# Kernel tuning notes

Hardware: AMD Instinct MI355X
Metric: run time of the kernel (lower is better)

## Reference

```python
import jax, jax.numpy as jnp
import numpy as np

N_IN, N_REC, T, BATCH = 128, 512, 1000, 64
ALPHA = 0.2
SIGMA = float(np.sqrt(2.0 / ALPHA) * 0.05)  # sqrt(2/alpha)*sigma_rec
EI_RATIO = 0.8
W_REC_GAIN = 1.0


def setup_inputs() -> dict:
    key = jax.random.key(0)
    k_x, k_n = jax.random.split(key)
    rng = np.random.RandomState(0)
    # w_in init: randn/sqrt(n_in)
    w_in = (rng.randn(N_IN, N_REC) / np.sqrt(N_IN)).astype(np.float32)
    # w_rec init 'randgauss' with Dale's law: abs, inhibitory rows scaled
    n_ex = int(N_REC * EI_RATIO)
    w_rec0 = W_REC_GAIN * rng.randn(N_REC, N_REC) / np.sqrt(N_REC)
    w_rec0 = np.abs(w_rec0)
    w_rec0[n_ex:, :] *= EI_RATIO / (1.0 - EI_RATIO)
    w_rec = w_rec0.astype(np.float32)
    ei_vec = np.concatenate([np.ones(n_ex), -np.ones(N_REC - n_ex)]).astype(np.float32)
    ei_mask = np.diag(ei_vec)
    autapse_mask = np.ones((N_REC, N_REC), dtype=np.float32)
    np.fill_diagonal(autapse_mask, 0.0)
    x = jax.random.normal(k_x, (BATCH, T, N_IN), dtype=jnp.float32)
    # pre-scaled noise: randn * sigma, one draw per timestep (matches torch.randn_like(h)*sigma)
    noise = jax.random.normal(k_n, (BATCH, T, N_REC), dtype=jnp.float32) * SIGMA
    return {
        "x": x,
        "w_in": jnp.asarray(w_in),
        "w_rec": jnp.asarray(w_rec),
        "b_rec": jnp.zeros((N_REC,), dtype=jnp.float32),
        "ei_mask": jnp.asarray(ei_mask),
        "autapse_mask": jnp.asarray(autapse_mask),
        "noise": noise,
    }


def reference(x, w_in, w_rec, b_rec, ei_mask, autapse_mask, noise):
    # Effective recurrent weight, computed ONCE (torch code recomputes each step)
    w_eff = ei_mask @ (w_rec * autapse_mask)          # (n_rec, n_rec)
    inp_all = jnp.einsum("bti,ir->btr", x, w_in)       # precompute input projection
    xs = (jnp.swapaxes(inp_all, 0, 1), jnp.swapaxes(noise, 0, 1))  # (T,b,r)
    h0 = jnp.zeros((x.shape[0], w_rec.shape[0]), dtype=x.dtype)

    def step(h, xt):
        inp_t, noise_t = xt
        pre = inp_t + h @ w_eff + b_rec + noise_t
        h_new = (1.0 - ALPHA) * h + ALPHA * jax.nn.relu(pre)
        return h_new, h_new

    _, h_all = jax.lax.scan(step, h0, xs)              # (T, batch, n_rec)
    return jnp.swapaxes(h_all, 0, 1)                   # (batch, T, n_rec)
```

## Files before the change

### kernel.cpp

```cpp
#include <hip/hip_runtime.h>

#define T_STEPS 1000
#define NIN     128
#define NREC    512
#define NBATCH  64
#define ALPHA   0.2f

#define NSLICE  4
#define SCOLS   128
#define NGRP    8
#define KPER    64

#define WS_W_OFF      0
#define WS_COMM_OFF   (1u << 20)
#define COMM_U64      (NBATCH * NREC)
#define COMM_BYTES    (2 * COMM_U64 * 8)
#define WS_COMM2_OFF  (WS_COMM_OFF + COMM_BYTES)
#define WS_NEEDED_LLC (WS_COMM_OFF + COMM_BYTES)
#define WS_NEEDED_DUAL (WS_COMM2_OFF + COMM_BYTES)

#define LDS_BARRIER() do {                                        \
    asm volatile("s_waitcnt lgkmcnt(0)" ::: "memory");            \
    __builtin_amdgcn_s_barrier();                                 \
    asm volatile("" ::: "memory");                                \
} while (0)

__device__ __forceinline__ unsigned long long ld_l2(
        const unsigned long long* p) {
    unsigned long long r;
    asm volatile("global_load_dwordx2 %0, %1, off sc0\n\t"
                 "s_waitcnt vmcnt(0)"
                 : "=v"(r) : "v"(p) : "memory");
    return r;
}
__device__ __forceinline__ void st_l2(unsigned long long* p,
                                      unsigned long long v) {
    asm volatile("global_store_dwordx2 %0, %1, off"
                 :: "v"(p), "v"(v) : "memory");
}
__device__ __forceinline__ unsigned long long ld_llc(
        const unsigned long long* p) {
    return __hip_atomic_load(p, __ATOMIC_RELAXED, __HIP_MEMORY_SCOPE_AGENT);
}
__device__ __forceinline__ void st_llc(unsigned long long* p,
                                       unsigned long long v) {
    __hip_atomic_store(p, v, __ATOMIC_RELAXED, __HIP_MEMORY_SCOPE_AGENT);
}

__global__ void weff_kernel(const float* __restrict__ w_rec,
                            const float* __restrict__ ei_mask,
                            const float* __restrict__ autapse,
                            float* __restrict__ w_eff) {
    int idx = blockIdx.x * blockDim.x + threadIdx.x;
    if (idx < NREC * NREC) {
        int row = idx >> 9;
        float ei = ei_mask[row * NREC + row];
        w_eff[idx] = ei * w_rec[idx] * autapse[idx];
    }
}

__global__ __launch_bounds__(1024) void gemm_in_kernel(
        const float* __restrict__ x,
        const float* __restrict__ w_in,
        const float* __restrict__ b_rec,
        float* __restrict__ io) {
    __shared__ float xs[32][NIN];

    const int tid = threadIdx.x;
    const int m0  = blockIdx.x * 32;

    {
        const float4* src = reinterpret_cast<const float4*>(x + (size_t)m0 * NIN);
        reinterpret_cast<float4*>(&xs[0][0])[tid] = src[tid];
    }
    __syncthreads();

    const int j0 = tid & 255;
    const int j1 = j0 + 256;
    const int rg = tid >> 8;

    float acc[8][2];
#pragma unroll
    for (int i = 0; i < 8; ++i) { acc[i][0] = 0.f; acc[i][1] = 0.f; }

#pragma unroll 4
    for (int k = 0; k < NIN; ++k) {
        float wv0 = w_in[k * NREC + j0];
        float wv1 = w_in[k * NREC + j1];
#pragma unroll
        for (int i = 0; i < 8; ++i) {
            float xv = xs[rg * 8 + i][k];
            acc[i][0] = fmaf(xv, wv0, acc[i][0]);
            acc[i][1] = fmaf(xv, wv1, acc[i][1]);
        }
    }

    const float br0 = b_rec[j0];
    const float br1 = b_rec[j1];
#pragma unroll
    for (int i = 0; i < 8; ++i) {
        size_t ro = (size_t)(m0 + rg * 8 + i) * NREC;
        io[ro + j0] = acc[i][0] + br0;
        io[ro + j1] = acc[i][1] + br1;
    }
}

__global__ __launch_bounds__(1024, 4) void rnn_coop(
        const float* __restrict__ W,
        const float* __restrict__ noise,
        float* __restrict__ io,
        unsigned long long* __restrict__ comm,
        unsigned long long* __restrict__ comm2) {
    __shared__ float h_own[SCOLS];
    __shared__ float part[NGRP][SCOLS];

    const int tid = threadIdx.x;
    const int bid = blockIdx.x;
    const int b   = (bid & 7) + 8 * (bid >> 5);
    const int s   = (bid >> 3) & 3;
    const int w   = tid >> 6;
    const int ln  = tid & 63;
    const int g   = w >> 1;
    const int c   = w & 1;
    const int col = c * 64 + ln;
    const int jg  = s * SCOLS + col;
    const bool own       = (w >> 2) == s;
    const bool is_leader = own && ((w & 2) == 0);
    const bool use_l2    = (comm2 != nullptr);

    float Wr[KPER];
    {
        const float* wp = W + (size_t)(g * KPER) * NREC + jg;
#pragma unroll
        for (int u = 0; u < KPER; ++u)
            Wr[u] = wp[(size_t)u * NREC];
    }
#pragma unroll
    for (int u = 0; u < KPER; ++u)
        asm volatile("" : "+v"(Wr[u]));

    float hj = 0.f;
    const size_t iobase = (size_t)b * T_STEPS * NREC + jg;
    const unsigned long long* cpoll  = comm  + (size_t)b * NREC + g * KPER + ln;
    const unsigned long long* cpoll2 = comm2 + (size_t)b * NREC + g * KPER + ln;
    unsigned long long* cwr  = comm  + (size_t)b * NREC + jg;
    unsigned long long* cwr2 = comm2 + (size_t)b * NREC + jg;

    float inp = 0.f, nz = 0.f;
    if (is_leader) { inp = io[iobase]; nz = noise[iobase]; }

    for (int t = 0; t < T_STEPS; ++t) {
        float hval;
        if (t == 0) {
            hval = 0.f;
        } else if (own) {
            hval = h_own[(g & 1) * KPER + ln];
        } else {
            const size_t po = (size_t)(t & 1) * COMM_U64;
            unsigned long long v;
            if (use_l2) {
                v = ld_l2(cpoll2 + po);
                while ((int)(unsigned)(v >> 32) < t) {
                    v = ld_llc(cpoll + po);
                    if ((int)(unsigned)(v >> 32) >= t) break;
                    v = ld_l2(cpoll2 + po);
                }
            } else {
                v = ld_llc(cpoll + po);
                while ((int)(unsigned)(v >> 32) < t)
                    v = ld_llc(cpoll + po);
            }
            hval = __uint_as_float((unsigned)(v & 0xffffffffu));
        }

        float a0 = 0.f, a1 = 0.f;
#pragma unroll
        for (int u = 0; u < KPER; u += 2) {
            float h0 = __uint_as_float(
                __builtin_amdgcn_readlane(__float_as_uint(hval), u));
            float h1 = __uint_as_float(
                __builtin_amdgcn_readlane(__float_as_uint(hval), u + 1));
            a0 = fmaf(h0, Wr[u],     a0);
            a1 = fmaf(h1, Wr[u + 1], a1);
        }
        part[g][col] = a0 + a1;
        LDS_BARRIER();

        if (is_leader) {
            float pre = inp + nz;
#pragma unroll
            for (int q = 0; q < NGRP; ++q)
                pre += part[q][col];
            float hnew = (1.f - ALPHA) * hj + ALPHA * fmaxf(pre, 0.f);
            hj = hnew;
            h_own[col] = hnew;
            unsigned long long pv =
                ((unsigned long long)(unsigned)(t + 1) << 32) |
                (unsigned long long)__float_as_uint(hnew);
            const size_t po = (size_t)((t + 1) & 1) * COMM_U64;
            if (use_l2) st_l2(cwr2 + po, pv);
            st_llc(cwr + po, pv);
            io[iobase + (size_t)t * NREC] = hnew;
            if (t + 1 < T_STEPS) {
                inp = io[iobase + (size_t)(t + 1) * NREC];
                nz  = noise[iobase + (size_t)(t + 1) * NREC];
            }
        }
        LDS_BARRIER();
    }
}

__global__ __launch_bounds__(1024) void rnn_kernel(
        const float* __restrict__ W,
        const float* __restrict__ noise,
        float* __restrict__ io) {
    __shared__ float h[NREC];
    __shared__ float part2[NREC];

    const int tid  = threadIdx.x;
    const int j    = tid & (NREC - 1);
    const int half = tid >> 9;
    const int b    = blockIdx.x;

    if (tid < NREC) h[tid] = 0.f;
    float hj = 0.f;
    __syncthreads();

    const int kb = half * 256;
    const float* wp = W + (size_t)kb * NREC + j;
    const size_t base = (size_t)b * T_STEPS * NREC + j;

    for (int t = 0; t < T_STEPS; ++t) {
        const size_t off = base + (size_t)t * NREC;
        float acc = (half == 0) ? (io[off] + noise[off]) : 0.f;
#pragma unroll
        for (int ku = 0; ku < 256; ku += 16) {
            float wv[16];
#pragma unroll
            for (int u = 0; u < 16; ++u) wv[u] = wp[(size_t)(ku + u) * NREC];
#pragma unroll
            for (int u = 0; u < 16; ++u) acc = fmaf(h[kb + ku + u], wv[u], acc);
        }
        if (half == 1) part2[j] = acc;
        __syncthreads();
        if (half == 0) {
            float pre  = acc + part2[j];
            float hnew = (1.f - ALPHA) * hj + ALPHA * fmaxf(pre, 0.f);
            io[off] = hnew;
            h[j] = hnew;
            hj = hnew;
        }
        __syncthreads();
    }
}

extern "C" void kernel_launch(void* const* d_in, const int* in_sizes, int n_in,
                              void* d_out, int out_size, void* d_ws, size_t ws_size,
                              hipStream_t stream) {
    const float* x       = (const float*)d_in[0];
    const float* w_in    = (const float*)d_in[1];
    const float* w_rec   = (const float*)d_in[2];
    const float* b_rec   = (const float*)d_in[3];
    const float* ei_mask = (const float*)d_in[4];
    const float* autapse = (const float*)d_in[5];
    const float* noise   = (const float*)d_in[6];
    float* out = (float*)d_out;

    char* ws = (char*)d_ws;
    float* W = (float*)(ws + WS_W_OFF);
    unsigned long long* comm  = (unsigned long long*)(ws + WS_COMM_OFF);
    unsigned long long* comm2 = (unsigned long long*)(ws + WS_COMM2_OFF);

    weff_kernel<<<dim3((NREC * NREC + 255) / 256), dim3(256), 0, stream>>>(
        w_rec, ei_mask, autapse, W);

    gemm_in_kernel<<<dim3(64000 / 32), dim3(1024), 0, stream>>>(
        x, w_in, b_rec, out);

    if (ws_size >= (size_t)WS_NEEDED_DUAL) {
        hipMemsetAsync(comm, 0, 2 * COMM_BYTES, stream);
        void* args[] = {(void*)&W, (void*)&noise, (void*)&out,
                        (void*)&comm, (void*)&comm2};
        hipLaunchCooperativeKernel(reinterpret_cast<void*>(rnn_coop),
                                   dim3(NBATCH * NSLICE), dim3(1024),
                                   args, 0, stream);
    } else if (ws_size >= (size_t)WS_NEEDED_LLC) {
        hipMemsetAsync(comm, 0, COMM_BYTES, stream);
        unsigned long long* nul = nullptr;
        void* args[] = {(void*)&W, (void*)&noise, (void*)&out,
                        (void*)&comm, (void*)&nul};
        hipLaunchCooperativeKernel(reinterpret_cast<void*>(rnn_coop),
                                   dim3(NBATCH * NSLICE), dim3(1024),
                                   args, 0, stream);
    } else {
        rnn_kernel<<<dim3(NBATCH), dim3(1024), 0, stream>>>(W, noise, out);
    }
}
```

Baseline: 1.676 ms.

## Replace per-step workgroup barriers with LDS flag-based point-to-point sync

Drops both s_barrier calls per timestep in the cooperative RNN kernel and instead double-buffers the partial sums and owned hidden state in LDS. Waves signal completion through per-wave LDS flags, and leader waves spin on those flags. The waves that produced an h slice reuse their own register value, and the next-step input and noise loads are issued before the leader waits. The goal is to cut barrier stalls on the serial critical path, at the cost of LDS spin-polling and reliance on relaxed LDS atomics for correct ordering.

```diff
diff --git a/kernel.cpp b/kernel.cpp
--- a/kernel.cpp
+++ b/kernel.cpp
@@ -19,12 +19,6 @@
 #define WS_NEEDED_LLC (WS_COMM_OFF + COMM_BYTES)
 #define WS_NEEDED_DUAL (WS_COMM2_OFF + COMM_BYTES)
 
-#define LDS_BARRIER() do {                                        \
-    asm volatile("s_waitcnt lgkmcnt(0)" ::: "memory");            \
-    __builtin_amdgcn_s_barrier();                                 \
-    asm volatile("" ::: "memory");                                \
-} while (0)
-
 __device__ __forceinline__ unsigned long long ld_l2(
         const unsigned long long* p) {
     unsigned long long r;
@@ -45,6 +39,9 @@
 __device__ __forceinline__ void st_llc(unsigned long long* p,
                                        unsigned long long v) {
     __hip_atomic_store(p, v, __ATOMIC_RELAXED, __HIP_MEMORY_SCOPE_AGENT);
+}
+__device__ __forceinline__ int ld_lds_i32(const int* p) {
+    return __hip_atomic_load(p, __ATOMIC_RELAXED, __HIP_MEMORY_SCOPE_WORKGROUP);
 }
 
 __global__ void weff_kernel(const float* __restrict__ w_rec,
@@ -111,8 +108,10 @@
         float* __restrict__ io,
         unsigned long long* __restrict__ comm,
         unsigned long long* __restrict__ comm2) {
-    __shared__ float h_own[SCOLS];
-    __shared__ float part[NGRP][SCOLS];
+    __shared__ float h_own[2][SCOLS];
+    __shared__ float part[2][NGRP][SCOLS];
+    __shared__ int   wflag[2][16];
+    __shared__ int   hflag[2][2];
 
     const int tid = threadIdx.x;
     const int bid = blockIdx.x;
@@ -124,8 +123,9 @@
     const int c   = w & 1;
     const int col = c * 64 + ln;
     const int jg  = s * SCOLS + col;
-    const bool own       = (w >> 2) == s;
+    const bool own       = (g >> 1) == s;
     const bool is_leader = own && ((w & 2) == 0);
+    const bool self_h    = is_leader && (c == 0);
     const bool use_l2    = (comm2 != nullptr);
 
     float Wr[KPER];
@@ -146,17 +146,27 @@
     unsigned long long* cwr  = comm  + (size_t)b * NREC + jg;
     unsigned long long* cwr2 = comm2 + (size_t)b * NREC + jg;
 
+    if (tid < 32) wflag[tid >> 4][tid & 15] = -1;
+    if (tid < 4)  hflag[tid >> 1][tid & 1] = 0;
     float inp = 0.f, nz = 0.f;
     if (is_leader) { inp = io[iobase]; nz = noise[iobase]; }
+    __syncthreads();
 
     for (int t = 0; t < T_STEPS; ++t) {
+        const int p = t & 1;
+
         float hval;
         if (t == 0) {
             hval = 0.f;
+        } else if (self_h) {
+            hval = hj;
         } else if (own) {
-            hval = h_own[(g & 1) * KPER + ln];
+            const int need = g & 1;
+            while (ld_lds_i32(&hflag[p][need]) < t) {}
+            asm volatile("" ::: "memory");
+            hval = h_own[p][need * 64 + ln];
         } else {
-            const size_t po = (size_t)(t & 1) * COMM_U64;
+            const size_t po = (size_t)p * COMM_U64;
             unsigned long long v;
             if (use_l2) {
                 v = ld_l2(cpoll2 + po);
@@ -183,30 +193,42 @@
             a0 = fmaf(h0, Wr[u],     a0);
             a1 = fmaf(h1, Wr[u + 1], a1);
         }
-        part[g][col] = a0 + a1;
-        LDS_BARRIER();
+
+        part[p][g][col] = a0 + a1;
+        asm volatile("s_waitcnt lgkmcnt(0)" ::: "memory");
+        if (ln == 0) wflag[p][w] = t;
 
         if (is_leader) {
+            float ninp = 0.f, nnz = 0.f;
+            if (t + 1 < T_STEPS) {
+                ninp = io[iobase + (size_t)(t + 1) * NREC];
+                nnz  = noise[iobase + (size_t)(t + 1) * NREC];
+            }
+            for (;;) {
+                int fv = ld_lds_i32(&wflag[p][ln & 15]);
+                if (__all(fv >= t)) break;
+            }
+            asm volatile("" ::: "memory");
             float pre = inp + nz;
 #pragma unroll
             for (int q = 0; q < NGRP; ++q)
-                pre += part[q][col];
+                pre += part[p][q][col];
             float hnew = (1.f - ALPHA) * hj + ALPHA * fmaxf(pre, 0.f);
             hj = hnew;
-            h_own[col] = hnew;
-            unsigned long long pv =
-                ((unsigned long long)(unsigned)(t + 1) << 32) |
-                (unsigned long long)__float_as_uint(hnew);
-            const size_t po = (size_t)((t + 1) & 1) * COMM_U64;
-            if (use_l2) st_l2(cwr2 + po, pv);
-            st_llc(cwr + po, pv);
+            if (t + 1 < T_STEPS) {
+                h_own[p ^ 1][col] = hnew;
+                asm volatile("s_waitcnt lgkmcnt(0)" ::: "memory");
+                if (ln == 0) hflag[p ^ 1][c] = t + 1;
+                unsigned long long pv =
+                    ((unsigned long long)(unsigned)(t + 1) << 32) |
+                    (unsigned long long)__float_as_uint(hnew);
+                const size_t po = (size_t)((t + 1) & 1) * COMM_U64;
+                if (use_l2) st_l2(cwr2 + po, pv);
+                st_llc(cwr + po, pv);
+            }
             io[iobase + (size_t)t * NREC] = hnew;
-            if (t + 1 < T_STEPS) {
-                inp = io[iobase + (size_t)(t + 1) * NREC];
-                nz  = noise[iobase + (size_t)(t + 1) * NREC];
-            }
-        }
-        LDS_BARRIER();
+            inp = ninp; nz = nnz;
+        }
     }
 }
 
```

Result: slower. 1.857 ms (+10.8%).
